# Kernel tuning notes

Hardware: AMD Instinct MI355X
Metric: run time of the kernel (lower is better)

## Reference

```python
import jax, jax.numpy as jnp
import numpy as np

N_NODES = 50000
N_EDGES = 800000
N_FEAT = 256


def setup_inputs() -> dict:
    key = jax.random.key(0)
    k_h, k_src, k_dst, k_w1, k_w2 = jax.random.split(key, 5)
    h = jax.random.normal(k_h, (N_NODES, N_FEAT), dtype=jnp.float32)
    src = jax.random.randint(k_src, (N_EDGES,), 0, N_NODES, dtype=jnp.int32)
    dst = jax.random.randint(k_dst, (N_EDGES,), 0, N_NODES, dtype=jnp.int32)
    # Kaiming-uniform-ish init like nn.Linear defaults
    b1 = 1.0 / np.sqrt(2 * N_FEAT)
    b2 = 1.0 / np.sqrt(N_FEAT)
    W1_w = jax.random.uniform(k_w1, (N_FEAT, 2 * N_FEAT), dtype=jnp.float32, minval=-b1, maxval=b1)
    W1_b = jnp.zeros((N_FEAT,), dtype=jnp.float32)
    W2_w = jax.random.uniform(k_w2, (1, N_FEAT), dtype=jnp.float32, minval=-b2, maxval=b2)
    W2_b = jnp.zeros((1,), dtype=jnp.float32)
    return {"h": h, "src": src, "dst": dst, "W1_w": W1_w, "W1_b": W1_b, "W2_w": W2_w, "W2_b": W2_b}


def reference(h, src, dst, W1_w, W1_b, W2_w, W2_b):
    # Gather per-edge endpoint features and concat along feature dim: [E, 2F]
    e = jnp.concatenate([h[src], h[dst]], axis=-1)
    # 2-layer MLP: Linear -> ReLU -> Linear, squeeze to per-edge score [E]
    hid = jax.nn.relu(e @ W1_w.T + W1_b)          # [E, F]
    score = (hid @ W2_w.T + W2_b)[:, 0]            # [E]
    return score
```

## Files before the change

kernel.cpp:

```cpp
#include <hip/hip_runtime.h>

#define F 256
#define TWO_F 512
#define BM 128
#define BN 64
#define BK 64

typedef __attribute__((ext_vector_type(8))) short short8;
typedef __attribute__((ext_vector_type(4))) float float4v;

static __device__ __forceinline__ unsigned short f2bf(float f) {
    unsigned u = __float_as_uint(f);
    u += 0x7FFFu + ((u >> 16) & 1u);
    return (unsigned short)(u >> 16);
}
static __device__ __forceinline__ unsigned pack2(float lo, float hi) {
    unsigned a = __float_as_uint(lo) + 0x8000u;
    unsigned b = __float_as_uint(hi) + 0x8000u;
    return __builtin_amdgcn_perm(b, a, 0x07060302u);
}
static __device__ __forceinline__ float blo(unsigned u) { return __uint_as_float(u << 16); }
static __device__ __forceinline__ float rawf(unsigned u) { return __uint_as_float(u); }

__global__ __launch_bounds__(256) void prep_kernel(
    const float* __restrict__ h, const float* __restrict__ W1,
    unsigned short* __restrict__ hb, unsigned short* __restrict__ Wb, int M)
{
    int i = blockIdx.x * blockDim.x + threadIdx.x;
    if (i < M * 128) {
        int m = i >> 7;
        int kp = (i & 127) * 2;
        float2 v = *(const float2*)(h + (size_t)m * F + kp);
        unsigned pk = pack2(v.x, v.y);
        int ksw = ((kp & 63) + (m & 7) * 8) & 63;
        *(unsigned*)(hb + (size_t)m * F + (kp & ~63) + ksw) = pk;
    }
    if (i < TWO_F * F) {
        int n = i >> 8;
        int k = i & 255;
        float v = W1[(n & 255) * TWO_F + ((n >> 8) << 8) + k];
        int kin_sw = ((k & 63) + (n & 7) * 8) & 63;
        Wb[n * F + (k & ~63) + kin_sw] = f2bf(v);
    }
}

__global__ __launch_bounds__(256, 4) void gemm_kernel(
    const unsigned short* __restrict__ hb, const unsigned short* __restrict__ Wb,
    const float* __restrict__ b1v, unsigned short* __restrict__ C, int M)
{
    __shared__ unsigned short sA[BM * BK];
    __shared__ unsigned short sB[BN * BK];

    const int ib = blockIdx.x;
    const int r8 = ib & 7;
    const int q  = ib >> 3;
    const int by = q & 7;
    const int bx = (q >> 3) * 8 + r8;
    const int bm = bx * BM;
    if (bm >= M) return;
    const int bn = by * BN;

    const int tid  = threadIdx.x;
    const int lane = tid & 63;
    const int wid  = tid >> 6;
    const int st_r = lane >> 3;
    const int st_k = (lane & 7) * 8;
    const int quad = lane >> 4;
    const int l15  = lane & 15;
    const int rot  = (l15 & 7) * 8;

    float4v acc[2][4];
    #pragma unroll
    for (int i = 0; i < 2; ++i)
        #pragma unroll
        for (int j = 0; j < 4; ++j) acc[i][j] = (float4v)(0.f);

    for (int k0 = 0; k0 < F; k0 += BK) {
        #pragma unroll
        for (int p = 0; p < 4; ++p) {
            int r = wid * 32 + p * 8;
            int am = bm + r + st_r; if (am > M - 1) am = M - 1;
            const unsigned short* ga = hb + (size_t)am * F + k0 + st_k;
            __builtin_amdgcn_global_load_lds(
                (const __attribute__((address_space(1))) unsigned int*)ga,
                (__attribute__((address_space(3))) unsigned int*)&sA[r * BK],
                16, 0, 0);
        }
        #pragma unroll
        for (int p = 0; p < 2; ++p) {
            int r = wid * 16 + p * 8;
            const unsigned short* gb = Wb + (size_t)(bn + r + st_r) * F + k0 + st_k;
            __builtin_amdgcn_global_load_lds(
                (const __attribute__((address_space(1))) unsigned int*)gb,
                (__attribute__((address_space(3))) unsigned int*)&sB[r * BK],
                16, 0, 0);
        }
        __syncthreads();

        #pragma unroll
        for (int ks = 0; ks < 2; ++ks) {
            const int koff = (ks * 32 + quad * 8 + rot) & 63;
            short8 afr[2], bfr[4];
            #pragma unroll
            for (int mt = 0; mt < 2; ++mt)
                afr[mt] = *(const short8*)&sA[(wid * 32 + mt * 16 + l15) * BK + koff];
            #pragma unroll
            for (int nt = 0; nt < 4; ++nt)
                bfr[nt] = *(const short8*)&sB[(nt * 16 + l15) * BK + koff];
            #pragma unroll
            for (int mt = 0; mt < 2; ++mt)
                #pragma unroll
                for (int nt = 0; nt < 4; ++nt)
                    acc[mt][nt] = __builtin_amdgcn_mfma_f32_16x16x32_bf16(
                        afr[mt], bfr[nt], acc[mt][nt], 0, 0, 0);
        }
        __syncthreads();
    }

    float bias[4];
    #pragma unroll
    for (int nt = 0; nt < 4; ++nt) {
        int n = bn + nt * 16 + l15;
        bias[nt] = (n < F) ? b1v[n] : 0.f;
    }
    #pragma unroll
    for (int mt = 0; mt < 2; ++mt) {
        #pragma unroll
        for (int rr = 0; rr < 4; ++rr) {
            int row = wid * 32 + mt * 16 + quad * 4 + rr;
            #pragma unroll
            for (int nt = 0; nt < 4; ++nt)
                sA[row * BK + nt * 16 + l15] = f2bf(acc[mt][nt][rr] + bias[nt]);
        }
    }
    __syncthreads();
    #pragma unroll
    for (int p = 0; p < 4; ++p) {
        int row = p * 32 + (tid >> 3);
        int gm = bm + row;
        if (gm < M) {
            uint4 v = *(const uint4*)&sA[row * BK + (tid & 7) * 8];
            *(uint4*)(C + (size_t)gm * TWO_F + bn + (tid & 7) * 8) = v;
        }
    }
}

__global__ __launch_bounds__(256) void edge_kernel(
    const unsigned short* __restrict__ C,
    const int* __restrict__ src, const int* __restrict__ dst,
    const float* __restrict__ w2,
    const float* __restrict__ b2, float* __restrict__ out, int E)
{
    const int lane = threadIdx.x & 31;
    const int g = blockIdx.x * 8 + (threadIdx.x >> 5);
    const int e0 = g * 2;
    if (e0 >= E) return;
    const int s0 = src[e0], d0 = dst[e0];
    const int s1 = src[e0 + 1], d1 = dst[e0 + 1];

    uint4 av0 = *(const uint4*)(C + (size_t)s0 * TWO_F + lane * 8);
    uint4 bv0 = *(const uint4*)(C + (size_t)d0 * TWO_F + F + lane * 8);
    uint4 av1 = *(const uint4*)(C + (size_t)s1 * TWO_F + lane * 8);
    uint4 bv1 = *(const uint4*)(C + (size_t)d1 * TWO_F + F + lane * 8);
    float4 w0 = *(const float4*)(w2 + lane * 8);
    float4 w1 = *(const float4*)(w2 + lane * 8 + 4);

    float sum0, sum1;
    sum0  = w0.x * fmaxf(blo(av0.x) + blo(bv0.x), 0.f);
    sum0 += w0.y * fmaxf(rawf(av0.x) + rawf(bv0.x), 0.f);
    sum0 += w0.z * fmaxf(blo(av0.y) + blo(bv0.y), 0.f);
    sum0 += w0.w * fmaxf(rawf(av0.y) + rawf(bv0.y), 0.f);
    sum0 += w1.x * fmaxf(blo(av0.z) + blo(bv0.z), 0.f);
    sum0 += w1.y * fmaxf(rawf(av0.z) + rawf(bv0.z), 0.f);
    sum0 += w1.z * fmaxf(blo(av0.w) + blo(bv0.w), 0.f);
    sum0 += w1.w * fmaxf(rawf(av0.w) + rawf(bv0.w), 0.f);

    sum1  = w0.x * fmaxf(blo(av1.x) + blo(bv1.x), 0.f);
    sum1 += w0.y * fmaxf(rawf(av1.x) + rawf(bv1.x), 0.f);
    sum1 += w0.z * fmaxf(blo(av1.y) + blo(bv1.y), 0.f);
    sum1 += w0.w * fmaxf(rawf(av1.y) + rawf(bv1.y), 0.f);
    sum1 += w1.x * fmaxf(blo(av1.z) + blo(bv1.z), 0.f);
    sum1 += w1.y * fmaxf(rawf(av1.z) + rawf(bv1.z), 0.f);
    sum1 += w1.z * fmaxf(blo(av1.w) + blo(bv1.w), 0.f);
    sum1 += w1.w * fmaxf(rawf(av1.w) + rawf(bv1.w), 0.f);

    #pragma unroll
    for (int off = 16; off > 0; off >>= 1) {
        sum0 += __shfl_down(sum0, off, 32);
        sum1 += __shfl_down(sum1, off, 32);
    }

    if (lane == 0) {
        float b = b2[0];
        out[e0]     = sum0 + b;
        out[e0 + 1] = sum1 + b;
    }
}

extern "C" void kernel_launch(void* const* d_in, const int* in_sizes, int n_in,
                              void* d_out, int out_size, void* d_ws, size_t ws_size,
                              hipStream_t stream) {
    const float* h    = (const float*)d_in[0];
    const int*   src  = (const int*)d_in[1];
    const int*   dst  = (const int*)d_in[2];
    const float* W1_w = (const float*)d_in[3];
    const float* W1_b = (const float*)d_in[4];
    const float* W2_w = (const float*)d_in[5];
    const float* W2_b = (const float*)d_in[6];
    float* out = (float*)d_out;

    const int M = in_sizes[0] / F;
    const int E = in_sizes[1];

    unsigned short* Wb = (unsigned short*)d_ws;
    unsigned short* hb = (unsigned short*)((char*)d_ws + 512 * 1024);
    unsigned short* C  = (unsigned short*)((char*)d_ws + 512 * 1024 + 26 * 1024 * 1024);

    int prep_threads = M * 128 > TWO_F * F ? M * 128 : TWO_F * F;
    prep_kernel<<<(prep_threads + 255) / 256, 256, 0, stream>>>(h, W1_w, hb, Wb, M);

    int nbx = ((M + BM - 1) / BM + 7) / 8 * 8;
    gemm_kernel<<<nbx * 8, 256, 0, stream>>>(hb, Wb, W1_b, C, M);

    edge_kernel<<<(E / 2 + 7) / 8, 256, 0, stream>>>(C, src, dst, W2_w, W2_b, out, E);
}
```

Baseline: 225.3 us.

## Bucket-sort edges by source, make GEMM persistent with resident W tile

The GEMM becomes a persistent kernel: each block keeps its full 64x256 W slice resident in LDS, double-buffers A tiles, and walks seven row strips. Edges are counting-sorted into buckets of 128 source nodes using histogram, scan and scatter kernels. The edge kernel reads the sorted (src,dst) pairs, which improves cache locality of the source-side gathers, and writes each score back to its original index. The cost is four extra small launches plus a memset, and an extra pass over src/dst. The sorted buffers reuse the hb workspace once the GEMM has finished with it.

```diff
diff --git a/kernel.cpp b/kernel.cpp
--- a/kernel.cpp
+++ b/kernel.cpp
@@ -5,6 +5,8 @@
 #define BM 128
 #define BN 64
 #define BK 64
+#define NITER 7
+#define NBKT 392
 
 typedef __attribute__((ext_vector_type(8))) short short8;
 typedef __attribute__((ext_vector_type(4))) float float4v;
@@ -44,21 +46,19 @@
     }
 }
 
-__global__ __launch_bounds__(256, 4) void gemm_kernel(
+__global__ __launch_bounds__(256, 2) void gemm_kernel(
     const unsigned short* __restrict__ hb, const unsigned short* __restrict__ Wb,
     const float* __restrict__ b1v, unsigned short* __restrict__ C, int M)
 {
-    __shared__ unsigned short sA[BM * BK];
-    __shared__ unsigned short sB[BN * BK];
-
-    const int ib = blockIdx.x;
-    const int r8 = ib & 7;
-    const int q  = ib >> 3;
-    const int by = q & 7;
-    const int bx = (q >> 3) * 8 + r8;
-    const int bm = bx * BM;
-    if (bm >= M) return;
-    const int bn = by * BN;
+    __shared__ unsigned short sB[BN * F];
+    __shared__ unsigned short sA[2][BM * BK];
+
+    const int ib  = blockIdx.x;
+    const int r8  = ib & 7;
+    const int t   = ib >> 3;
+    const int bxg = (t % 7) * 8 + r8;
+    const int by  = t / 7;
+    const int bn  = by * BN;
 
     const int tid  = threadIdx.x;
     const int lane = tid & 63;
@@ -69,99 +69,160 @@
     const int l15  = lane & 15;
     const int rot  = (l15 & 7) * 8;
 
-    float4v acc[2][4];
-    #pragma unroll
-    for (int i = 0; i < 2; ++i)
-        #pragma unroll
-        for (int j = 0; j < 4; ++j) acc[i][j] = (float4v)(0.f);
-
-    for (int k0 = 0; k0 < F; k0 += BK) {
+    #pragma unroll
+    for (int p = 0; p < 8; ++p) {
+        int r = wid * 16 + p * 2;
+        const unsigned short* gb = Wb + (size_t)(bn + r) * F + lane * 8;
+        __builtin_amdgcn_global_load_lds(
+            (const __attribute__((address_space(1))) unsigned int*)gb,
+            (__attribute__((address_space(3))) unsigned int*)&sB[r * F],
+            16, 0, 0);
+    }
+
+    float bias[4];
+    #pragma unroll
+    for (int nt = 0; nt < 4; ++nt) {
+        int n = bn + nt * 16 + l15;
+        bias[nt] = (n < F) ? b1v[n] : 0.f;
+    }
+
+    auto stageA = [&](int buf, int bm_, int k0) {
         #pragma unroll
         for (int p = 0; p < 4; ++p) {
             int r = wid * 32 + p * 8;
-            int am = bm + r + st_r; if (am > M - 1) am = M - 1;
+            int am = bm_ + r + st_r; if (am > M - 1) am = M - 1;
             const unsigned short* ga = hb + (size_t)am * F + k0 + st_k;
             __builtin_amdgcn_global_load_lds(
                 (const __attribute__((address_space(1))) unsigned int*)ga,
-                (__attribute__((address_space(3))) unsigned int*)&sA[r * BK],
+                (__attribute__((address_space(3))) unsigned int*)&sA[buf][r * BK],
                 16, 0, 0);
         }
-        #pragma unroll
-        for (int p = 0; p < 2; ++p) {
-            int r = wid * 16 + p * 8;
-            const unsigned short* gb = Wb + (size_t)(bn + r + st_r) * F + k0 + st_k;
-            __builtin_amdgcn_global_load_lds(
-                (const __attribute__((address_space(1))) unsigned int*)gb,
-                (__attribute__((address_space(3))) unsigned int*)&sB[r * BK],
-                16, 0, 0);
-        }
-        __syncthreads();
-
-        #pragma unroll
-        for (int ks = 0; ks < 2; ++ks) {
-            const int koff = (ks * 32 + quad * 8 + rot) & 63;
-            short8 afr[2], bfr[4];
+    };
+
+    for (int it = 0; it < NITER; ++it) {
+        const int strip = bxg * NITER + it;
+        const int bm = strip * BM;
+        if (bm >= M) break;
+
+        float4v acc[2][4];
+        #pragma unroll
+        for (int i = 0; i < 2; ++i)
             #pragma unroll
-            for (int mt = 0; mt < 2; ++mt)
-                afr[mt] = *(const short8*)&sA[(wid * 32 + mt * 16 + l15) * BK + koff];
+            for (int j = 0; j < 4; ++j) acc[i][j] = (float4v)(0.f);
+
+        stageA(0, bm, 0);
+        __syncthreads();
+
+        #pragma unroll
+        for (int kt = 0; kt < 4; ++kt) {
+            const int cur = kt & 1;
+            if (kt < 3) stageA(cur ^ 1, bm, (kt + 1) * BK);
+
             #pragma unroll
-            for (int nt = 0; nt < 4; ++nt)
-                bfr[nt] = *(const short8*)&sB[(nt * 16 + l15) * BK + koff];
+            for (int ks = 0; ks < 2; ++ks) {
+                const int koff = (ks * 32 + quad * 8 + rot) & 63;
+                short8 afr[2], bfr[4];
+                #pragma unroll
+                for (int mt = 0; mt < 2; ++mt)
+                    afr[mt] = *(const short8*)&sA[cur][(wid * 32 + mt * 16 + l15) * BK + koff];
+                #pragma unroll
+                for (int nt = 0; nt < 4; ++nt)
+                    bfr[nt] = *(const short8*)&sB[(nt * 16 + l15) * F + kt * BK + koff];
+                #pragma unroll
+                for (int mt = 0; mt < 2; ++mt)
+                    #pragma unroll
+                    for (int nt = 0; nt < 4; ++nt)
+                        acc[mt][nt] = __builtin_amdgcn_mfma_f32_16x16x32_bf16(
+                            afr[mt], bfr[nt], acc[mt][nt], 0, 0, 0);
+            }
+            __syncthreads();
+        }
+
+        #pragma unroll
+        for (int mt = 0; mt < 2; ++mt) {
             #pragma unroll
-            for (int mt = 0; mt < 2; ++mt)
+            for (int rr = 0; rr < 4; ++rr) {
+                int row = wid * 32 + mt * 16 + quad * 4 + rr;
                 #pragma unroll
                 for (int nt = 0; nt < 4; ++nt)
-                    acc[mt][nt] = __builtin_amdgcn_mfma_f32_16x16x32_bf16(
-                        afr[mt], bfr[nt], acc[mt][nt], 0, 0, 0);
-        }
-        __syncthreads();
-    }
-
-    float bias[4];
-    #pragma unroll
-    for (int nt = 0; nt < 4; ++nt) {
-        int n = bn + nt * 16 + l15;
-        bias[nt] = (n < F) ? b1v[n] : 0.f;
-    }
-    #pragma unroll
-    for (int mt = 0; mt < 2; ++mt) {
-        #pragma unroll
-        for (int rr = 0; rr < 4; ++rr) {
-            int row = wid * 32 + mt * 16 + quad * 4 + rr;
-            #pragma unroll
-            for (int nt = 0; nt < 4; ++nt)
-                sA[row * BK + nt * 16 + l15] = f2bf(acc[mt][nt][rr] + bias[nt]);
-        }
-    }
+                    sA[0][row * BK + nt * 16 + l15] = f2bf(acc[mt][nt][rr] + bias[nt]);
+            }
+        }
+        __syncthreads();
+        #pragma unroll
+        for (int p = 0; p < 4; ++p) {
+            int row = p * 32 + (tid >> 3);
+            int gm = bm + row;
+            if (gm < M) {
+                uint4 v = *(const uint4*)&sA[0][row * BK + (tid & 7) * 8];
+                *(uint4*)(C + (size_t)gm * TWO_F + bn + (tid & 7) * 8) = v;
+            }
+        }
+        __syncthreads();
+    }
+}
+
+__global__ __launch_bounds__(256) void hist_kernel(
+    const int* __restrict__ src, int* __restrict__ counts, int E)
+{
+    int i = blockIdx.x * 256 + threadIdx.x;
+    if (i < E) atomicAdd(&counts[((unsigned)src[i]) >> 7], 1);
+}
+
+__global__ void scan_kernel(const int* __restrict__ counts, int* __restrict__ cursor)
+{
+    __shared__ int s[512];
+    int tid = threadIdx.x;
+    int v = (tid < NBKT) ? counts[tid] : 0;
+    s[tid] = v;
     __syncthreads();
     #pragma unroll
-    for (int p = 0; p < 4; ++p) {
-        int row = p * 32 + (tid >> 3);
-        int gm = bm + row;
-        if (gm < M) {
-            uint4 v = *(const uint4*)&sA[row * BK + (tid & 7) * 8];
-            *(uint4*)(C + (size_t)gm * TWO_F + bn + (tid & 7) * 8) = v;
-        }
+    for (int off = 1; off < 512; off <<= 1) {
+        int x = (tid >= off) ? s[tid - off] : 0;
+        __syncthreads();
+        s[tid] += x;
+        __syncthreads();
+    }
+    if (tid < NBKT) cursor[tid] = s[tid] - v;
+}
+
+__global__ __launch_bounds__(256) void scatter_kernel(
+    const int* __restrict__ src, const int* __restrict__ dst,
+    int* __restrict__ cursor, int2* __restrict__ sort_sd,
+    int* __restrict__ sort_idx, int E)
+{
+    int i = blockIdx.x * 256 + threadIdx.x;
+    if (i < E) {
+        int s = src[i];
+        int pos = atomicAdd(&cursor[((unsigned)s) >> 7], 1);
+        sort_sd[pos] = make_int2(s, dst[i]);
+        sort_idx[pos] = i;
     }
 }
 
 __global__ __launch_bounds__(256) void edge_kernel(
     const unsigned short* __restrict__ C,
-    const int* __restrict__ src, const int* __restrict__ dst,
+    const int2* __restrict__ sd, const int* __restrict__ sidx,
     const float* __restrict__ w2,
     const float* __restrict__ b2, float* __restrict__ out, int E)
 {
     const int lane = threadIdx.x & 31;
-    const int g = blockIdx.x * 8 + (threadIdx.x >> 5);
+    const int nblk = gridDim.x;
+    const int ib = blockIdx.x;
+    const int gb = (nblk & 7) == 0 ? ((ib & 7) * (nblk >> 3) + (ib >> 3)) : ib;
+    const int g = gb * 8 + (threadIdx.x >> 5);
     const int e0 = g * 2;
     if (e0 >= E) return;
-    const int s0 = src[e0], d0 = dst[e0];
-    const int s1 = src[e0 + 1], d1 = dst[e0 + 1];
-
-    uint4 av0 = *(const uint4*)(C + (size_t)s0 * TWO_F + lane * 8);
-    uint4 bv0 = *(const uint4*)(C + (size_t)d0 * TWO_F + F + lane * 8);
-    uint4 av1 = *(const uint4*)(C + (size_t)s1 * TWO_F + lane * 8);
-    uint4 bv1 = *(const uint4*)(C + (size_t)d1 * TWO_F + F + lane * 8);
+    const bool has1 = (e0 + 1 < E);
+    int2 p0 = sd[e0];
+    int2 p1 = has1 ? sd[e0 + 1] : p0;
+    int i0 = sidx[e0];
+    int i1 = has1 ? sidx[e0 + 1] : 0;
+
+    uint4 av0 = *(const uint4*)(C + (size_t)p0.x * TWO_F + lane * 8);
+    uint4 bv0 = *(const uint4*)(C + (size_t)p0.y * TWO_F + F + lane * 8);
+    uint4 av1 = *(const uint4*)(C + (size_t)p1.x * TWO_F + lane * 8);
+    uint4 bv1 = *(const uint4*)(C + (size_t)p1.y * TWO_F + F + lane * 8);
     float4 w0 = *(const float4*)(w2 + lane * 8);
     float4 w1 = *(const float4*)(w2 + lane * 8 + 4);
 
@@ -192,8 +253,8 @@
 
     if (lane == 0) {
         float b = b2[0];
-        out[e0]     = sum0 + b;
-        out[e0 + 1] = sum1 + b;
+        out[i0] = sum0 + b;
+        if (has1) out[i1] = sum1 + b;
     }
 }
 
@@ -215,12 +276,21 @@
     unsigned short* Wb = (unsigned short*)d_ws;
     unsigned short* hb = (unsigned short*)((char*)d_ws + 512 * 1024);
     unsigned short* C  = (unsigned short*)((char*)d_ws + 512 * 1024 + 26 * 1024 * 1024);
+    int2* sort_sd  = (int2*)hb;
+    int*  sort_idx = (int*)((char*)hb + 8 * 1024 * 1024);
+    int*  counts   = (int*)((char*)hb + 12 * 1024 * 1024);
+    int*  cursor   = counts + 512;
 
     int prep_threads = M * 128 > TWO_F * F ? M * 128 : TWO_F * F;
     prep_kernel<<<(prep_threads + 255) / 256, 256, 0, stream>>>(h, W1_w, hb, Wb, M);
 
-    int nbx = ((M + BM - 1) / BM + 7) / 8 * 8;
-    gemm_kernel<<<nbx * 8, 256, 0, stream>>>(hb, Wb, W1_b, C, M);
-
-    edge_kernel<<<(E / 2 + 7) / 8, 256, 0, stream>>>(C, src, dst, W2_w, W2_b, out, E);
-}
+    gemm_kernel<<<56 * 8, 256, 0, stream>>>(hb, Wb, W1_b, C, M);
+
+    hipMemsetAsync(counts, 0, 2 * 512 * sizeof(int), stream);
+    hist_kernel<<<(E + 255) / 256, 256, 0, stream>>>(src, counts, E);
+    scan_kernel<<<1, 512, 0, stream>>>(counts, cursor);
+    scatter_kernel<<<(E + 255) / 256, 256, 0, stream>>>(src, dst, cursor, sort_sd, sort_idx, E);
+
+    int eblocks = (E / 2 + 7) / 8;
+    edge_kernel<<<eblocks, 256, 0, stream>>>(C, sort_sd, sort_idx, W2_w, W2_b, out, E);
+}
```

After: 763.6 us. +238.9%, slower.

## Bucket-sort edges by source and double-buffer GEMM LDS tiles

Applied to the files above, without the earlier changes.

Adds a three-kernel counting sort that buckets edges by source node (128-node buckets), so the edge kernel gathers C rows with better locality and scatters scores back through a stored permutation. The edge kernel's block indices are also remapped in an XCD-aware order. Separately, the GEMM now double-buffers its LDS tiles, prefetching the next K tile during the MFMAs and dropping one barrier per iteration, with occupancy lowered to 3 blocks per SM. The sort adds three launches, a single-block scan and scattered writes. The sort buffers reuse the hb workspace after the GEMM, which is safe only because of stream ordering.

```diff
diff --git a/kernel.cpp b/kernel.cpp
--- a/kernel.cpp
+++ b/kernel.cpp
@@ -5,6 +5,8 @@
 #define BM 128
 #define BN 64
 #define BK 64
+#define NBKT 512
+#define EPB 4096
 
 typedef __attribute__((ext_vector_type(8))) short short8;
 typedef __attribute__((ext_vector_type(4))) float float4v;
@@ -44,12 +46,12 @@
     }
 }
 
-__global__ __launch_bounds__(256, 4) void gemm_kernel(
+__global__ __launch_bounds__(256, 3) void gemm_kernel(
     const unsigned short* __restrict__ hb, const unsigned short* __restrict__ Wb,
     const float* __restrict__ b1v, unsigned short* __restrict__ C, int M)
 {
-    __shared__ unsigned short sA[BM * BK];
-    __shared__ unsigned short sB[BN * BK];
+    __shared__ unsigned short sA[2][BM * BK];
+    __shared__ unsigned short sB[2][BN * BK];
 
     const int ib = blockIdx.x;
     const int r8 = ib & 7;
@@ -75,7 +77,7 @@
         #pragma unroll
         for (int j = 0; j < 4; ++j) acc[i][j] = (float4v)(0.f);
 
-    for (int k0 = 0; k0 < F; k0 += BK) {
+    auto stage = [&](int buf, int k0) {
         #pragma unroll
         for (int p = 0; p < 4; ++p) {
             int r = wid * 32 + p * 8;
@@ -83,7 +85,7 @@
             const unsigned short* ga = hb + (size_t)am * F + k0 + st_k;
             __builtin_amdgcn_global_load_lds(
                 (const __attribute__((address_space(1))) unsigned int*)ga,
-                (__attribute__((address_space(3))) unsigned int*)&sA[r * BK],
+                (__attribute__((address_space(3))) unsigned int*)&sA[buf][r * BK],
                 16, 0, 0);
         }
         #pragma unroll
@@ -92,10 +94,18 @@
             const unsigned short* gb = Wb + (size_t)(bn + r + st_r) * F + k0 + st_k;
             __builtin_amdgcn_global_load_lds(
                 (const __attribute__((address_space(1))) unsigned int*)gb,
-                (__attribute__((address_space(3))) unsigned int*)&sB[r * BK],
+                (__attribute__((address_space(3))) unsigned int*)&sB[buf][r * BK],
                 16, 0, 0);
         }
+    };
+
+    stage(0, 0);
+
+    #pragma unroll
+    for (int kt = 0; kt < 4; ++kt) {
+        const int cur = kt & 1;
         __syncthreads();
+        if (kt < 3) stage(cur ^ 1, (kt + 1) * BK);
 
         #pragma unroll
         for (int ks = 0; ks < 2; ++ks) {
@@ -103,10 +113,10 @@
             short8 afr[2], bfr[4];
             #pragma unroll
             for (int mt = 0; mt < 2; ++mt)
-                afr[mt] = *(const short8*)&sA[(wid * 32 + mt * 16 + l15) * BK + koff];
+                afr[mt] = *(const short8*)&sA[cur][(wid * 32 + mt * 16 + l15) * BK + koff];
             #pragma unroll
             for (int nt = 0; nt < 4; ++nt)
-                bfr[nt] = *(const short8*)&sB[(nt * 16 + l15) * BK + koff];
+                bfr[nt] = *(const short8*)&sB[cur][(nt * 16 + l15) * BK + koff];
             #pragma unroll
             for (int mt = 0; mt < 2; ++mt)
                 #pragma unroll
@@ -114,7 +124,6 @@
                     acc[mt][nt] = __builtin_amdgcn_mfma_f32_16x16x32_bf16(
                         afr[mt], bfr[nt], acc[mt][nt], 0, 0, 0);
         }
-        __syncthreads();
     }
 
     float bias[4];
@@ -130,7 +139,7 @@
             int row = wid * 32 + mt * 16 + quad * 4 + rr;
             #pragma unroll
             for (int nt = 0; nt < 4; ++nt)
-                sA[row * BK + nt * 16 + l15] = f2bf(acc[mt][nt][rr] + bias[nt]);
+                sA[0][row * BK + nt * 16 + l15] = f2bf(acc[mt][nt][rr] + bias[nt]);
         }
     }
     __syncthreads();
@@ -139,29 +148,110 @@
         int row = p * 32 + (tid >> 3);
         int gm = bm + row;
         if (gm < M) {
-            uint4 v = *(const uint4*)&sA[row * BK + (tid & 7) * 8];
+            uint4 v = *(const uint4*)&sA[0][row * BK + (tid & 7) * 8];
             *(uint4*)(C + (size_t)gm * TWO_F + bn + (tid & 7) * 8) = v;
+        }
+    }
+}
+
+__global__ __launch_bounds__(256) void sort_count_kernel(
+    const int* __restrict__ src, int* __restrict__ counts, int E)
+{
+    __shared__ int cnt[NBKT];
+    const int tid = threadIdx.x;
+    #pragma unroll
+    for (int i = tid; i < NBKT; i += 256) cnt[i] = 0;
+    __syncthreads();
+    const int base = blockIdx.x * EPB;
+    #pragma unroll
+    for (int j = 0; j < EPB / 256; ++j) {
+        int e = base + j * 256 + tid;
+        if (e < E) atomicAdd(&cnt[((unsigned)src[e]) >> 7], 1);
+    }
+    __syncthreads();
+    #pragma unroll
+    for (int i = tid; i < NBKT; i += 256) counts[blockIdx.x * NBKT + i] = cnt[i];
+}
+
+__global__ __launch_bounds__(512) void sort_scan_kernel(
+    int* __restrict__ counts, int* __restrict__ bucketbase, int nsb)
+{
+    __shared__ int s[NBKT];
+    const int tid = threadIdx.x;
+    int run = 0;
+    int blk = 0;
+    for (; blk + 8 <= nsb; blk += 8) {
+        int v[8];
+        #pragma unroll
+        for (int u = 0; u < 8; ++u) v[u] = counts[(blk + u) * NBKT + tid];
+        #pragma unroll
+        for (int u = 0; u < 8; ++u) { counts[(blk + u) * NBKT + tid] = run; run += v[u]; }
+    }
+    for (; blk < nsb; ++blk) {
+        int v = counts[blk * NBKT + tid];
+        counts[blk * NBKT + tid] = run;
+        run += v;
+    }
+    s[tid] = run;
+    __syncthreads();
+    #pragma unroll
+    for (int off = 1; off < NBKT; off <<= 1) {
+        int x = (tid >= off) ? s[tid - off] : 0;
+        __syncthreads();
+        s[tid] += x;
+        __syncthreads();
+    }
+    bucketbase[tid] = s[tid] - run;
+}
+
+__global__ __launch_bounds__(256) void sort_scatter_kernel(
+    const int* __restrict__ src, const int* __restrict__ dst,
+    const int* __restrict__ counts, const int* __restrict__ bucketbase,
+    int2* __restrict__ sort_sd, int* __restrict__ sort_idx, int E)
+{
+    __shared__ int cnt[NBKT];
+    const int tid = threadIdx.x;
+    #pragma unroll
+    for (int i = tid; i < NBKT; i += 256) cnt[i] = 0;
+    __syncthreads();
+    const int base = blockIdx.x * EPB;
+    #pragma unroll
+    for (int j = 0; j < EPB / 256; ++j) {
+        int e = base + j * 256 + tid;
+        if (e < E) {
+            int s = src[e];
+            int b = ((unsigned)s) >> 7;
+            int r = atomicAdd(&cnt[b], 1);
+            int pos = bucketbase[b] + counts[blockIdx.x * NBKT + b] + r;
+            sort_sd[pos] = make_int2(s, dst[e]);
+            sort_idx[pos] = e;
         }
     }
 }
 
 __global__ __launch_bounds__(256) void edge_kernel(
     const unsigned short* __restrict__ C,
-    const int* __restrict__ src, const int* __restrict__ dst,
+    const int2* __restrict__ sd, const int* __restrict__ sidx,
     const float* __restrict__ w2,
     const float* __restrict__ b2, float* __restrict__ out, int E)
 {
     const int lane = threadIdx.x & 31;
-    const int g = blockIdx.x * 8 + (threadIdx.x >> 5);
+    const int nblk = gridDim.x;
+    const int ib = blockIdx.x;
+    const int gb = (nblk & 7) == 0 ? ((ib & 7) * (nblk >> 3) + (ib >> 3)) : ib;
+    const int g = gb * 8 + (threadIdx.x >> 5);
     const int e0 = g * 2;
     if (e0 >= E) return;
-    const int s0 = src[e0], d0 = dst[e0];
-    const int s1 = src[e0 + 1], d1 = dst[e0 + 1];
-
-    uint4 av0 = *(const uint4*)(C + (size_t)s0 * TWO_F + lane * 8);
-    uint4 bv0 = *(const uint4*)(C + (size_t)d0 * TWO_F + F + lane * 8);
-    uint4 av1 = *(const uint4*)(C + (size_t)s1 * TWO_F + lane * 8);
-    uint4 bv1 = *(const uint4*)(C + (size_t)d1 * TWO_F + F + lane * 8);
+    const bool has1 = (e0 + 1 < E);
+    int2 p0 = sd[e0];
+    int2 p1 = has1 ? sd[e0 + 1] : p0;
+    int i0 = sidx[e0];
+    int i1 = has1 ? sidx[e0 + 1] : 0;
+
+    uint4 av0 = *(const uint4*)(C + (size_t)p0.x * TWO_F + lane * 8);
+    uint4 bv0 = *(const uint4*)(C + (size_t)p0.y * TWO_F + F + lane * 8);
+    uint4 av1 = *(const uint4*)(C + (size_t)p1.x * TWO_F + lane * 8);
+    uint4 bv1 = *(const uint4*)(C + (size_t)p1.y * TWO_F + F + lane * 8);
     float4 w0 = *(const float4*)(w2 + lane * 8);
     float4 w1 = *(const float4*)(w2 + lane * 8 + 4);
 
@@ -192,8 +282,8 @@
 
     if (lane == 0) {
         float b = b2[0];
-        out[e0]     = sum0 + b;
-        out[e0 + 1] = sum1 + b;
+        out[i0] = sum0 + b;
+        if (has1) out[i1] = sum1 + b;
     }
 }
 
@@ -215,6 +305,10 @@
     unsigned short* Wb = (unsigned short*)d_ws;
     unsigned short* hb = (unsigned short*)((char*)d_ws + 512 * 1024);
     unsigned short* C  = (unsigned short*)((char*)d_ws + 512 * 1024 + 26 * 1024 * 1024);
+    int2* sort_sd    = (int2*)hb;
+    int*  sort_idx   = (int*)((char*)hb + 8 * 1024 * 1024);
+    int*  counts     = (int*)((char*)hb + 12 * 1024 * 1024);
+    int*  bucketbase = (int*)((char*)hb + 13 * 1024 * 1024);
 
     int prep_threads = M * 128 > TWO_F * F ? M * 128 : TWO_F * F;
     prep_kernel<<<(prep_threads + 255) / 256, 256, 0, stream>>>(h, W1_w, hb, Wb, M);
@@ -222,5 +316,11 @@
     int nbx = ((M + BM - 1) / BM + 7) / 8 * 8;
     gemm_kernel<<<nbx * 8, 256, 0, stream>>>(hb, Wb, W1_b, C, M);
 
-    edge_kernel<<<(E / 2 + 7) / 8, 256, 0, stream>>>(C, src, dst, W2_w, W2_b, out, E);
-}
+    int nsb = (E + EPB - 1) / EPB;
+    sort_count_kernel<<<nsb, 256, 0, stream>>>(src, counts, E);
+    sort_scan_kernel<<<1, 512, 0, stream>>>(counts, bucketbase, nsb);
+    sort_scatter_kernel<<<nsb, 256, 0, stream>>>(src, dst, counts, bucketbase, sort_sd, sort_idx, E);
+
+    int eblocks = (E / 2 + 7) / 8;
+    edge_kernel<<<eblocks, 256, 0, stream>>>(C, sort_sd, sort_idx, W2_w, W2_b, out, E);
+}
```

After: 243.2 us. 1.08x slower.
